# Optimization experiments

Hardware: AMD Instinct MI355X
Metric: run time of the kernel (lower is better)

## Reference

```python
import jax, jax.numpy as jnp
import numpy as np

N = 5
C = 256
B, H, W = 8, 64, 64


def setup_inputs() -> dict:
    key = jax.random.key(0)
    ks = jax.random.split(key, 9)
    s = 0.05
    return {
        "inputs": jax.random.normal(ks[0], (B, N, C, H, W), dtype=jnp.float32),
        # grouped 1x1 conv: groups = N-1, each group maps C channels -> 1 channel, no bias
        "wgt_w": jax.random.normal(ks[1], (N - 1, C), dtype=jnp.float32) * s,
        # ConvGRU 1x1 gate convs: in = 2*C (cat of input and hidden), out = C, with bias
        "w_r": jax.random.normal(ks[2], (C, 2 * C), dtype=jnp.float32) * s,
        "b_r": jnp.zeros((C,), dtype=jnp.float32),
        "w_u": jax.random.normal(ks[3], (C, 2 * C), dtype=jnp.float32) * s,
        "b_u": jnp.zeros((C,), dtype=jnp.float32),
        "w_o": jax.random.normal(ks[4], (C, 2 * C), dtype=jnp.float32) * s,
        "b_o": jnp.zeros((C,), dtype=jnp.float32),
        "gamma": jax.random.normal(ks[5], (1,), dtype=jnp.float32) * s,
    }


def _conv1x1(x, Wm, bias):
    # x: [b, cin, h, w]; Wm: [cout, cin]
    return jnp.einsum("bchw,oc->bohw", x, Wm) + bias[None, :, None, None]


def reference(inputs, wgt_w, w_r, b_r, w_u, b_u, w_o, b_o, gamma):
    b, n, c, h, w = inputs.shape

    def gru(x, hprev):
        s = jnp.concatenate([x, hprev], axis=1)  # [b, 2c, h, w]
        u = jax.nn.sigmoid(_conv1x1(s, w_u, b_u))
        r = jax.nn.sigmoid(_conv1x1(s, w_r, b_r))
        o = jnp.tanh(_conv1x1(jnp.concatenate([x, hprev * r], axis=1), w_o, b_o))
        return hprev * (1.0 - u) + o * u

    preds = []
    for i in range(n):
        h_t = inputs[:, i]  # [b, c, h, w]
        idx = [j for j in range(n) if j != i]
        h_n = inputs[:, jnp.array(idx)]  # [b, n-1, c, h, w], neighbor-major channel layout
        diff = h_t[:, None] - h_n  # repeat(h_t, n-1) - cat(neighbors)
        # grouped 1x1 conv (groups = n-1, no bias): per-neighbor channel reduction
        wgt = jnp.einsum("bjchw,jc->bjhw", diff, wgt_w)  # [b, n-1, h, w]
        gate = jax.nn.sigmoid(wgt)
        # torch: wgt.unsqueeze(1).repeat(1, c, 1, 1, 1).view(b, c*(n-1), h, w)
        # -> flat channel index = cc*(n-1) + j  (note: differs from x2's j*c + cc layout)
        gate_full = jnp.broadcast_to(gate[:, None], (b, c, n - 1, h, w)).reshape(
            b, c * (n - 1), h, w
        )
        x2 = h_n.reshape(b, (n - 1) * c, h, w)
        msg = x2 * gate_full
        m_t = msg.reshape(b, n - 1, c, h, w).sum(axis=1)  # sum-aggregate over neighbors
        h_new = gru(m_t, h_t)
        preds.append(h_new * gamma + h_t)
    return jnp.stack(preds, axis=1)  # [b, n, c, h, w]
```

## Files before the change

### kernel.cpp

```cpp
#include <hip/hip_runtime.h>

typedef __attribute__((ext_vector_type(8))) short short8;
typedef __attribute__((ext_vector_type(4))) float f32x4;
typedef __attribute__((ext_vector_type(8))) unsigned short us8;
typedef __attribute__((ext_vector_type(4))) unsigned short us4;
typedef __attribute__((ext_vector_type(2))) unsigned short us2;

__device__ __forceinline__ float sigmoidf_(float x){ return 1.f/(1.f+__expf(-x)); }
__device__ __forceinline__ unsigned short f2bf(float f){
    union{float f; unsigned int u;} x; x.f = f;
    unsigned int r = x.u + 0x7fffu + ((x.u>>16)&1u);
    return (unsigned short)(r>>16);
}
__device__ __forceinline__ float bf2f(unsigned short u){
    union{unsigned int u; float f;} x; x.u = ((unsigned int)u)<<16; return x.f;
}
#define GAS(p) ((const __attribute__((address_space(1))) void*)(uintptr_t)(p))
#define LAS(p) ((__attribute__((address_space(3))) void*)(uintptr_t)(p))

#define SLOT 8388608ull

__global__ __launch_bounds__(256) void k_dots(const float* __restrict__ inp, const float* __restrict__ wgt,
                                              float* __restrict__ D){
    __shared__ float wg[1024];
    for (int s=threadIdx.x; s<1024; s+=256) wg[s] = wgt[s];
    __syncthreads();
    int e = blockIdx.x*256 + threadIdx.x;
    int pl = e & 4095;
    int bn = e >> 12;
    const float* base = inp + (((size_t)bn*256)<<12) + pl;
    float d0=0,d1=0,d2=0,d3=0;
    #pragma unroll 8
    for (int c=0;c<256;c++){
        float v = base[(size_t)c<<12];
        d0 += v*wg[c]; d1 += v*wg[256+c]; d2 += v*wg[512+c]; d3 += v*wg[768+c];
    }
    size_t o = ((size_t)bn*4)<<12;
    D[o+pl]=d0; D[o+4096+pl]=d1; D[o+8192+pl]=d2; D[o+12288+pl]=d3;
}

__global__ __launch_bounds__(256) void k_wp2(const float* __restrict__ w_u, const float* __restrict__ w_r,
                                             const float* __restrict__ w_o,
                                             unsigned short* __restrict__ Wc0, unsigned short* __restrict__ Wc1){
    int bx = blockIdx.x;
    const float *s0, *s1; unsigned short* dst; int OCN, tid;
    if (bx < 256){ tid = bx*256 + threadIdx.x; OCN = 512; s0 = w_u; s1 = w_r; dst = Wc0; }
    else         { tid = (bx-256)*256 + threadIdx.x; OCN = 256; s0 = w_o; s1 = w_o; dst = Wc1; }
    int d = tid*4;
    int kk = d & 63;
    int row = d >> 6;
    int oc = row & (OCN-1);
    int kb = row / OCN;
    int k  = kb*64 + kk;
    const float* src = (oc < 256) ? s0 : s1;
    int ocr = (oc < 256) ? oc : oc-256;
    float4 v = *(const float4*)&src[(size_t)ocr*512 + k];
    us4 pk; pk.x=f2bf(v.x); pk.y=f2bf(v.y); pk.z=f2bf(v.z); pk.w=f2bf(v.w);
    int kk_sw = kk ^ ((oc&7)<<3);
    *(us4*)&dst[(size_t)row*64 + kk_sw] = pk;
}

__global__ __launch_bounds__(256) void k_bxs(const float* __restrict__ inp, const float* __restrict__ D,
                                             unsigned short* __restrict__ Alo, unsigned short* __restrict__ Ahi,
                                             int i0, int cnt){
    __shared__ unsigned short tm[64*34];
    __shared__ unsigned short th[64*34];
    int t  = threadIdx.x;
    int c0 = (blockIdx.x & 3) << 6;
    int pz = blockIdx.x >> 2;
    int p0 = pz << 5;
    int b  = p0 >> 12, pl0 = p0 & 4095;

    f32x4 x[5][2], S4[2];
    #pragma unroll
    for (int q=0;q<2;q++){
        int s = t + q*256;
        int c = s >> 3, pc = (s&7) << 2;
        int cc = c0 + c;
        f32x4 acc = {0.f,0.f,0.f,0.f};
        #pragma unroll
        for (int n=0;n<5;n++){
            x[n][q] = *(const f32x4*)&inp[(((size_t)((b*5+n)*256+cc))<<12) + pl0 + pc];
            acc += x[n][q];
        }
        S4[q] = acc;
    }
    int kb = c0 >> 6;
    #pragma unroll
    for (int i=0;i<5;i++){
        if (i < i0 || i >= i0+cnt) continue;
        #pragma unroll
        for (int q=0;q<2;q++){
            int s = t + q*256;
            int c = s >> 3, pc = (s&7) << 2;
            int j = c & 3;
            int node = (j < i) ? j : (j+1);
            f32x4 dw = *(const f32x4*)&D[(((size_t)((b*5+i)*4+j))<<12) + pl0 + pc];
            f32x4 dn = *(const f32x4*)&D[(((size_t)((b*5+node)*4+j))<<12) + pl0 + pc];
            f32x4 xi = x[i][q];
            f32x4 md = S4[q] - xi;
            int lb = c*34 + pc;
            us2 m0, m1, h0, h1;
            m0.x = f2bf(sigmoidf_(dw.x-dn.x)*md.x); m0.y = f2bf(sigmoidf_(dw.y-dn.y)*md.y);
            m1.x = f2bf(sigmoidf_(dw.z-dn.z)*md.z); m1.y = f2bf(sigmoidf_(dw.w-dn.w)*md.w);
            h0.x = f2bf(xi.x); h0.y = f2bf(xi.y); h1.x = f2bf(xi.z); h1.y = f2bf(xi.w);
            *(us2*)&tm[lb] = m0; *(us2*)&tm[lb+2] = m1;
            *(us2*)&th[lb] = h0; *(us2*)&th[lb+2] = h1;
        }
        __syncthreads();
        {
            int p = t >> 3, cs = (t&7) << 3;
            us8 vm, vh;
            #pragma unroll
            for (int j8=0;j8<8;j8++){ vm[j8] = tm[(cs+j8)*34 + p]; vh[j8] = th[(cs+j8)*34 + p]; }
            int cs_sw = cs ^ ((p&7)<<3);
            size_t dst = (size_t)(i - i0)*SLOT + ((size_t)kb*32768 + p0 + p)*64 + cs_sw;
            *(us8*)&Alo[dst] = vm;
            *(us8*)&Ahi[dst] = vh;
        }
        __syncthreads();
    }
}

template<int EPI>
__global__ __launch_bounds__(256) void k_mm(
        const unsigned short* __restrict__ Alo, const unsigned short* __restrict__ Ahi,
        const unsigned short* __restrict__ Wb,
        const float* __restrict__ inp, const float* __restrict__ b0, const float* __restrict__ b1,
        unsigned short* __restrict__ U, unsigned short* __restrict__ A1hi, float* __restrict__ outp,
        const float* __restrict__ gamma_p, int i0)
{
    constexpr int OCN = EPI ? 256 : 512;
    constexpr int NY  = EPI ? 2   : 4;
    constexpr int NWG = 256*NY;
    __shared__ unsigned short As[2][128*64];
    __shared__ unsigned short Bs[2][128*64];
    int t  = threadIdx.x, wv = t>>6, ln = t&63;

    int bid = blockIdx.x;
    int wg  = (bid&7)*(NWG>>3) + (bid>>3);
    int oc0 = (wg & (NY-1)) * 128;
    int p0  = (wg / NY) * 128;

    int z  = blockIdx.z, i = i0 + z;
    size_t zo = (size_t)z*SLOT;
    int wm = (wv>>1)*64, wn = (wv&1)*64;
    int row = ln & 15, quad = ln >> 4, kq = quad*8;

    f32x4 acc[4][4];
    f32x4 zr = {0.f,0.f,0.f,0.f};
    #pragma unroll
    for (int a=0;a<4;a++){
        #pragma unroll
        for (int o=0;o<4;o++) acc[a][o]=zr;
    }

    auto stage = [&](int kb, int buf){
        const unsigned short* gA = (kb<4) ? (Alo + zo + ((size_t)kb*32768 + p0)*64)
                                          : (Ahi + zo + ((size_t)(kb-4)*32768 + p0)*64);
        const unsigned short* gW = Wb + ((size_t)kb*OCN + oc0)*64;
        #pragma unroll
        for (int q=0;q<4;q++){
            int off = (wv*4+q)*512;
            __builtin_amdgcn_global_load_lds(GAS(gA + off + ln*8), LAS(&Bs[buf][off + ln*8]), 16, 0, 0);
            __builtin_amdgcn_global_load_lds(GAS(gW + off + ln*8), LAS(&As[buf][off + ln*8]), 16, 0, 0);
        }
    };

    stage(0, 0);
    __syncthreads();

    int rsw = (row&7)<<3;
    for (int kb=0; kb<8; ++kb){
        int cur = kb & 1;
        if (kb < 7) stage(kb+1, cur^1);
        #pragma unroll
        for (int ks=0; ks<2; ks++){
            short8 a[4], b[4];
            int col = (ks*32 + kq) ^ rsw;
            #pragma unroll
            for (int f=0; f<4; f++){
                a[f] = *(const short8*)&As[cur][(wm+f*16+row)*64 + col];
                b[f] = *(const short8*)&Bs[cur][(wn+f*16+row)*64 + col];
            }
            __builtin_amdgcn_s_setprio(1);
            #pragma unroll
            for (int fm=0; fm<4; fm++){
                #pragma unroll
                for (int fn=0; fn<4; fn++)
                    acc[fm][fn] = __builtin_amdgcn_mfma_f32_16x16x32_bf16(a[fm], b[fn], acc[fm][fn], 0,0,0);
            }
            __builtin_amdgcn_s_setprio(0);
        }
        __syncthreads();
    }

    float gm = EPI ? gamma_p[0] : 0.f;
    #pragma unroll
    for (int fn=0; fn<4; fn++){
        int p  = p0 + wn + fn*16 + row;
        int b  = p >> 12, pl = p & 4095;
        size_t hb = (((size_t)((b*5+i)*256))<<12) + pl;
        #pragma unroll
        for (int fm=0; fm<4; fm++){
            int ocb = oc0 + wm + fm*16 + quad*4;
            if (EPI==0){
                if (oc0 < 256){
                    us4 pk;
                    #pragma unroll
                    for (int r=0;r<4;r++)
                        pk[r] = f2bf(sigmoidf_(acc[fm][fn][r] + b0[ocb+r]));
                    *(us4*)&U[zo + (size_t)p*256 + ocb] = pk;
                } else {
                    int kb2 = ocb - 256;
                    int kc  = (kb2&63) ^ ((p&7)<<3);
                    size_t aidx = zo + ((size_t)(kb2>>6)*32768 + p)*64 + kc;
                    us4 vh = *(const us4*)&Ahi[aidx];
                    us4 pk;
                    #pragma unroll
                    for (int r=0;r<4;r++){
                        float rg = sigmoidf_(acc[fm][fn][r] + b1[kb2+r]);
                        pk[r] = f2bf(rg * bf2f(vh[r]));
                    }
                    *(us4*)&A1hi[aidx] = pk;
                }
            } else {
                us4 vu = *(const us4*)&U[zo + (size_t)p*256 + ocb];
                #pragma unroll
                for (int r=0;r<4;r++){
                    int oc = ocb + r;
                    float v  = acc[fm][fn][r] + b0[oc];
                    float e2 = __expf(2.f*v);
                    float thv = 1.f - 2.f/(e2+1.f);
                    float u  = bf2f(vu[r]);
                    float h  = inp[hb + ((size_t)oc<<12)];
                    float hn = h*(1.f-u) + thv*u;
                    outp[hb + ((size_t)oc<<12)] = hn*gm + h;
                }
            }
        }
    }
}

extern "C" void kernel_launch(void* const* d_in, const int* in_sizes, int n_in,
                              void* d_out, int out_size, void* d_ws, size_t ws_size,
                              hipStream_t stream) {
    const float* inputs = (const float*)d_in[0];
    const float* wgt_w  = (const float*)d_in[1];
    const float* w_r    = (const float*)d_in[2];
    const float* b_r    = (const float*)d_in[3];
    const float* w_u    = (const float*)d_in[4];
    const float* b_u    = (const float*)d_in[5];
    const float* w_o    = (const float*)d_in[6];
    const float* b_o    = (const float*)d_in[7];
    const float* gamma  = (const float*)d_in[8];
    float* out = (float*)d_out;

    float* D = (float*)d_ws;
    unsigned short* Wc0 = (unsigned short*)(D + 655360);
    unsigned short* Wc1 = Wc0 + 262144;
    unsigned short* U   = Wc1 + 131072;

    size_t fixedB = 655360ull*4 + (262144ull + 131072ull)*2;
    size_t slotB  = 4ull*SLOT*2;
    int nb = 1;
    for (int k2=5;k2>=1;k2--){ if (fixedB + (size_t)k2*slotB <= ws_size){ nb = k2; break; } }

    unsigned short* Alo  = U   + (size_t)nb*SLOT;
    unsigned short* Ahi  = Alo + (size_t)nb*SLOT;
    unsigned short* A1hi = Ahi + (size_t)nb*SLOT;

    k_dots<<<640, 256, 0, stream>>>(inputs, wgt_w, D);
    k_wp2 <<<384, 256, 0, stream>>>(w_u, w_r, w_o, Wc0, Wc1);
    for (int i0=0; i0<5; i0+=nb){
        int cnt = (5-i0 < nb) ? (5-i0) : nb;
        k_bxs<<<4096, 256, 0, stream>>>(inputs, D, Alo, Ahi, i0, cnt);
        k_mm<0><<<dim3(1024,1,cnt), 256, 0, stream>>>(Alo, Ahi, Wc0, inputs, b_u, b_r,
                                                      U, A1hi, nullptr, gamma, i0);
        k_mm<1><<<dim3(512,1,cnt), 256, 0, stream>>>(Alo, A1hi, Wc1, inputs, b_o, nullptr,
                                                     U, nullptr, out, gamma, i0);
    }
}
```

Before: 707.6 us.

## Fuse gate dot products into message builder and make GEMMs persistent

Removes the separate k_dots kernel: each message-building block now computes the per-pixel neighbor dot products for its 32 pixels in shared memory before building the bf16 operand tiles, eliminating the D workspace round trip. Each block now covers all four channel tiles of its pixels, so the grid shrinks from 4096 to 1024 blocks. The GEMM kernels become persistent with 256 blocks, each looping over several output tiles with a 3-stage global-to-LDS pipeline using explicit vmcnt waits and running the epilogue inside the loop. The U intermediate uses a tile-contiguous layout for coalesced epilogue stores. This trades launch overhead and extra memory traffic for recomputing the dot products per node in every block, higher LDS use per block, and fewer resident blocks.

New measurement: 753.5 us. 1.06x slower.

```diff
diff --git a/kernel.cpp b/kernel.cpp
--- a/kernel.cpp
+++ b/kernel.cpp
@@ -19,25 +19,6 @@
 #define LAS(p) ((__attribute__((address_space(3))) void*)(uintptr_t)(p))
 
 #define SLOT 8388608ull
-
-__global__ __launch_bounds__(256) void k_dots(const float* __restrict__ inp, const float* __restrict__ wgt,
-                                              float* __restrict__ D){
-    __shared__ float wg[1024];
-    for (int s=threadIdx.x; s<1024; s+=256) wg[s] = wgt[s];
-    __syncthreads();
-    int e = blockIdx.x*256 + threadIdx.x;
-    int pl = e & 4095;
-    int bn = e >> 12;
-    const float* base = inp + (((size_t)bn*256)<<12) + pl;
-    float d0=0,d1=0,d2=0,d3=0;
-    #pragma unroll 8
-    for (int c=0;c<256;c++){
-        float v = base[(size_t)c<<12];
-        d0 += v*wg[c]; d1 += v*wg[256+c]; d2 += v*wg[512+c]; d3 += v*wg[768+c];
-    }
-    size_t o = ((size_t)bn*4)<<12;
-    D[o+pl]=d0; D[o+4096+pl]=d1; D[o+8192+pl]=d2; D[o+12288+pl]=d3;
-}
 
 __global__ __launch_bounds__(256) void k_wp2(const float* __restrict__ w_u, const float* __restrict__ w_r,
                                              const float* __restrict__ w_o,
@@ -60,65 +41,95 @@
     *(us4*)&dst[(size_t)row*64 + kk_sw] = pk;
 }
 
-__global__ __launch_bounds__(256) void k_bxs(const float* __restrict__ inp, const float* __restrict__ D,
-                                             unsigned short* __restrict__ Alo, unsigned short* __restrict__ Ahi,
-                                             int i0, int cnt){
+__global__ __launch_bounds__(256) void k_bxsd(const float* __restrict__ inp, const float* __restrict__ wgt,
+                                              unsigned short* __restrict__ Alo, unsigned short* __restrict__ Ahi,
+                                              int i0, int cnt){
+    __shared__ float wg[1024];
+    __shared__ float dpart[8*640];
+    __shared__ float Dl[640];
     __shared__ unsigned short tm[64*34];
     __shared__ unsigned short th[64*34];
     int t  = threadIdx.x;
-    int c0 = (blockIdx.x & 3) << 6;
-    int pz = blockIdx.x >> 2;
-    int p0 = pz << 5;
+    int p0 = blockIdx.x << 5;
     int b  = p0 >> 12, pl0 = p0 & 4095;
-
-    f32x4 x[5][2], S4[2];
-    #pragma unroll
-    for (int q=0;q<2;q++){
-        int s = t + q*256;
-        int c = s >> 3, pc = (s&7) << 2;
-        int cc = c0 + c;
-        f32x4 acc = {0.f,0.f,0.f,0.f};
-        #pragma unroll
-        for (int n=0;n<5;n++){
-            x[n][q] = *(const f32x4*)&inp[(((size_t)((b*5+n)*256+cc))<<12) + pl0 + pc];
-            acc += x[n][q];
-        }
-        S4[q] = acc;
-    }
-    int kb = c0 >> 6;
-    #pragma unroll
-    for (int i=0;i<5;i++){
-        if (i < i0 || i >= i0+cnt) continue;
+    for (int s=t; s<1024; s+=256) wg[s] = wgt[s];
+    __syncthreads();
+    {
+        int px = t & 31, cg = t >> 5;
+        float d[20];
+        #pragma unroll
+        for (int o=0;o<20;o++) d[o]=0.f;
+        #pragma unroll
+        for (int cc=0; cc<32; cc++){
+            int c = cg*32 + cc;
+            float w0 = wg[c], w1 = wg[256+c], w2 = wg[512+c], w3 = wg[768+c];
+            #pragma unroll
+            for (int n=0;n<5;n++){
+                float v = inp[(((size_t)((b*5+n)*256+c))<<12) + pl0 + px];
+                d[n*4+0] += v*w0; d[n*4+1] += v*w1; d[n*4+2] += v*w2; d[n*4+3] += v*w3;
+            }
+        }
+        #pragma unroll
+        for (int o=0;o<20;o++) dpart[cg*640 + o*32 + px] = d[o];
+    }
+    __syncthreads();
+    for (int o=t; o<640; o+=256){
+        float s = 0.f;
+        #pragma unroll
+        for (int g=0; g<8; g++) s += dpart[g*640 + o];
+        Dl[o] = s;
+    }
+    __syncthreads();
+    for (int ct=0; ct<4; ct++){
+        int c0 = ct << 6;
+        f32x4 x[5][2], S4[2];
         #pragma unroll
         for (int q=0;q<2;q++){
             int s = t + q*256;
             int c = s >> 3, pc = (s&7) << 2;
-            int j = c & 3;
-            int node = (j < i) ? j : (j+1);
-            f32x4 dw = *(const f32x4*)&D[(((size_t)((b*5+i)*4+j))<<12) + pl0 + pc];
-            f32x4 dn = *(const f32x4*)&D[(((size_t)((b*5+node)*4+j))<<12) + pl0 + pc];
-            f32x4 xi = x[i][q];
-            f32x4 md = S4[q] - xi;
-            int lb = c*34 + pc;
-            us2 m0, m1, h0, h1;
-            m0.x = f2bf(sigmoidf_(dw.x-dn.x)*md.x); m0.y = f2bf(sigmoidf_(dw.y-dn.y)*md.y);
-            m1.x = f2bf(sigmoidf_(dw.z-dn.z)*md.z); m1.y = f2bf(sigmoidf_(dw.w-dn.w)*md.w);
-            h0.x = f2bf(xi.x); h0.y = f2bf(xi.y); h1.x = f2bf(xi.z); h1.y = f2bf(xi.w);
-            *(us2*)&tm[lb] = m0; *(us2*)&tm[lb+2] = m1;
-            *(us2*)&th[lb] = h0; *(us2*)&th[lb+2] = h1;
-        }
-        __syncthreads();
-        {
-            int p = t >> 3, cs = (t&7) << 3;
-            us8 vm, vh;
-            #pragma unroll
-            for (int j8=0;j8<8;j8++){ vm[j8] = tm[(cs+j8)*34 + p]; vh[j8] = th[(cs+j8)*34 + p]; }
-            int cs_sw = cs ^ ((p&7)<<3);
-            size_t dst = (size_t)(i - i0)*SLOT + ((size_t)kb*32768 + p0 + p)*64 + cs_sw;
-            *(us8*)&Alo[dst] = vm;
-            *(us8*)&Ahi[dst] = vh;
-        }
-        __syncthreads();
+            int cc = c0 + c;
+            f32x4 acc = {0.f,0.f,0.f,0.f};
+            #pragma unroll
+            for (int n=0;n<5;n++){
+                x[n][q] = *(const f32x4*)&inp[(((size_t)((b*5+n)*256+cc))<<12) + pl0 + pc];
+                acc += x[n][q];
+            }
+            S4[q] = acc;
+        }
+        #pragma unroll
+        for (int i=0;i<5;i++){
+            if (i < i0 || i >= i0+cnt) continue;
+            #pragma unroll
+            for (int q=0;q<2;q++){
+                int s = t + q*256;
+                int c = s >> 3, pc = (s&7) << 2;
+                int j = c & 3;
+                int node = (j < i) ? j : (j+1);
+                f32x4 dw = *(const f32x4*)&Dl[(i*4+j)*32 + pc];
+                f32x4 dn = *(const f32x4*)&Dl[(node*4+j)*32 + pc];
+                f32x4 xi = x[i][q];
+                f32x4 md = S4[q] - xi;
+                int lb = c*34 + pc;
+                us2 m0, m1, h0, h1;
+                m0.x = f2bf(sigmoidf_(dw.x-dn.x)*md.x); m0.y = f2bf(sigmoidf_(dw.y-dn.y)*md.y);
+                m1.x = f2bf(sigmoidf_(dw.z-dn.z)*md.z); m1.y = f2bf(sigmoidf_(dw.w-dn.w)*md.w);
+                h0.x = f2bf(xi.x); h0.y = f2bf(xi.y); h1.x = f2bf(xi.z); h1.y = f2bf(xi.w);
+                *(us2*)&tm[lb] = m0; *(us2*)&tm[lb+2] = m1;
+                *(us2*)&th[lb] = h0; *(us2*)&th[lb+2] = h1;
+            }
+            __syncthreads();
+            {
+                int p = t >> 3, cs = (t&7) << 3;
+                us8 vm, vh;
+                #pragma unroll
+                for (int j8=0;j8<8;j8++){ vm[j8] = tm[(cs+j8)*34 + p]; vh[j8] = th[(cs+j8)*34 + p]; }
+                int cs_sw = cs ^ ((p&7)<<3);
+                size_t dst = (size_t)(i - i0)*SLOT + ((size_t)ct*32768 + p0 + p)*64 + cs_sw;
+                *(us8*)&Alo[dst] = vm;
+                *(us8*)&Ahi[dst] = vh;
+            }
+            __syncthreads();
+        }
     }
 }
 
@@ -128,24 +139,22 @@
         const unsigned short* __restrict__ Wb,
         const float* __restrict__ inp, const float* __restrict__ b0, const float* __restrict__ b1,
         unsigned short* __restrict__ U, unsigned short* __restrict__ A1hi, float* __restrict__ outp,
-        const float* __restrict__ gamma_p, int i0)
+        const float* __restrict__ gamma_p, int i0, int cnt)
 {
     constexpr int OCN = EPI ? 256 : 512;
     constexpr int NY  = EPI ? 2   : 4;
-    constexpr int NWG = 256*NY;
-    __shared__ unsigned short As[2][128*64];
-    __shared__ unsigned short Bs[2][128*64];
+    __shared__ unsigned short As[3][128*64];
+    __shared__ unsigned short Bs[3][128*64];
     int t  = threadIdx.x, wv = t>>6, ln = t&63;
-
-    int bid = blockIdx.x;
-    int wg  = (bid&7)*(NWG>>3) + (bid>>3);
-    int oc0 = (wg & (NY-1)) * 128;
-    int p0  = (wg / NY) * 128;
-
-    int z  = blockIdx.z, i = i0 + z;
-    size_t zo = (size_t)z*SLOT;
+    int NU = 256*NY*cnt;
+    int NS = (NU >> 8) * 8;
+    int chunk = blockIdx.x >> 5, k_in = blockIdx.x & 31;
+    int ubase = chunk*(NU>>3) + k_in;
+    int oc0 = (ubase & (NY-1)) * 128;
     int wm = (wv>>1)*64, wn = (wv&1)*64;
     int row = ln & 15, quad = ln >> 4, kq = quad*8;
+    int rsw = (row&7)<<3;
+    float gm = EPI ? gamma_p[0] : 0.f;
 
     f32x4 acc[4][4];
     f32x4 zr = {0.f,0.f,0.f,0.f};
@@ -155,10 +164,17 @@
         for (int o=0;o<4;o++) acc[a][o]=zr;
     }
 
-    auto stage = [&](int kb, int buf){
-        const unsigned short* gA = (kb<4) ? (Alo + zo + ((size_t)kb*32768 + p0)*64)
-                                          : (Ahi + zo + ((size_t)(kb-4)*32768 + p0)*64);
+    auto stage = [&](int s){
+        if (s >= NS) return;
+        int u  = ubase + (s>>3)*32;
+        int pz = u / NY;
+        int kb = s & 7;
+        int p0s = (pz & 255) << 7;
+        size_t zos = (size_t)(pz >> 8) * SLOT;
+        const unsigned short* gA = (kb<4) ? (Alo + zos + ((size_t)kb*32768 + p0s)*64)
+                                          : (Ahi + zos + ((size_t)(kb-4)*32768 + p0s)*64);
         const unsigned short* gW = Wb + ((size_t)kb*OCN + oc0)*64;
+        int buf = s % 3;
         #pragma unroll
         for (int q=0;q<4;q++){
             int off = (wv*4+q)*512;
@@ -167,13 +183,14 @@
         }
     };
 
-    stage(0, 0);
-    __syncthreads();
-
-    int rsw = (row&7)<<3;
-    for (int kb=0; kb<8; ++kb){
-        int cur = kb & 1;
-        if (kb < 7) stage(kb+1, cur^1);
+    stage(0); stage(1);
+    for (int s=0; s<NS; ++s){
+        if (s+1 < NS) { asm volatile("s_waitcnt vmcnt(8)" ::: "memory"); }
+        else          { asm volatile("s_waitcnt vmcnt(0)" ::: "memory"); }
+        __builtin_amdgcn_s_barrier();
+        __builtin_amdgcn_sched_barrier(0);
+        stage(s+2);
+        const int cur = s % 3;
         #pragma unroll
         for (int ks=0; ks<2; ks++){
             short8 a[4], b[4];
@@ -183,60 +200,85 @@
                 a[f] = *(const short8*)&As[cur][(wm+f*16+row)*64 + col];
                 b[f] = *(const short8*)&Bs[cur][(wn+f*16+row)*64 + col];
             }
-            __builtin_amdgcn_s_setprio(1);
             #pragma unroll
             for (int fm=0; fm<4; fm++){
                 #pragma unroll
                 for (int fn=0; fn<4; fn++)
                     acc[fm][fn] = __builtin_amdgcn_mfma_f32_16x16x32_bf16(a[fm], b[fn], acc[fm][fn], 0,0,0);
             }
-            __builtin_amdgcn_s_setprio(0);
-        }
-        __syncthreads();
-    }
-
-    float gm = EPI ? gamma_p[0] : 0.f;
-    #pragma unroll
-    for (int fn=0; fn<4; fn++){
-        int p  = p0 + wn + fn*16 + row;
-        int b  = p >> 12, pl = p & 4095;
-        size_t hb = (((size_t)((b*5+i)*256))<<12) + pl;
-        #pragma unroll
-        for (int fm=0; fm<4; fm++){
-            int ocb = oc0 + wm + fm*16 + quad*4;
+        }
+        if ((s&7)==7){
+            int u  = ubase + (s>>3)*32;
+            int pz = u / NY;
+            int p0 = (pz & 255) << 7;
+            int z  = pz >> 8;
+            size_t zo = (size_t)z*SLOT;
+            int i  = i0 + z;
             if (EPI==0){
                 if (oc0 < 256){
-                    us4 pk;
+                    size_t ub = zo + (size_t)((p0>>7)*2 + (oc0>>7))*16384 + (size_t)t*4;
                     #pragma unroll
-                    for (int r=0;r<4;r++)
-                        pk[r] = f2bf(sigmoidf_(acc[fm][fn][r] + b0[ocb+r]));
-                    *(us4*)&U[zo + (size_t)p*256 + ocb] = pk;
+                    for (int fn=0; fn<4; fn++){
+                        #pragma unroll
+                        for (int fm=0; fm<4; fm++){
+                            int ocb = oc0 + wm + fm*16 + quad*4;
+                            us4 pk;
+                            #pragma unroll
+                            for (int r=0;r<4;r++)
+                                pk[r] = f2bf(sigmoidf_(acc[fm][fn][r] + b0[ocb+r]));
+                            *(us4*)&U[ub + (size_t)(fn*4+fm)*1024] = pk;
+                        }
+                    }
                 } else {
-                    int kb2 = ocb - 256;
-                    int kc  = (kb2&63) ^ ((p&7)<<3);
-                    size_t aidx = zo + ((size_t)(kb2>>6)*32768 + p)*64 + kc;
-                    us4 vh = *(const us4*)&Ahi[aidx];
-                    us4 pk;
                     #pragma unroll
-                    for (int r=0;r<4;r++){
-                        float rg = sigmoidf_(acc[fm][fn][r] + b1[kb2+r]);
-                        pk[r] = f2bf(rg * bf2f(vh[r]));
+                    for (int fn=0; fn<4; fn++){
+                        int p = p0 + wn + fn*16 + row;
+                        #pragma unroll
+                        for (int fm=0; fm<4; fm++){
+                            int ocb = oc0 + wm + fm*16 + quad*4;
+                            int kb2 = ocb - 256;
+                            int kc  = (kb2&63) ^ ((p&7)<<3);
+                            size_t aidx = zo + ((size_t)(kb2>>6)*32768 + p)*64 + kc;
+                            us4 vh = *(const us4*)&Ahi[aidx];
+                            us4 pk;
+                            #pragma unroll
+                            for (int r=0;r<4;r++){
+                                float rg = sigmoidf_(acc[fm][fn][r] + b1[kb2+r]);
+                                pk[r] = f2bf(rg * bf2f(vh[r]));
+                            }
+                            *(us4*)&A1hi[aidx] = pk;
+                        }
                     }
-                    *(us4*)&A1hi[aidx] = pk;
                 }
             } else {
-                us4 vu = *(const us4*)&U[zo + (size_t)p*256 + ocb];
+                size_t ub = zo + (size_t)((p0>>7)*2 + (oc0>>7))*16384 + (size_t)t*4;
                 #pragma unroll
-                for (int r=0;r<4;r++){
-                    int oc = ocb + r;
-                    float v  = acc[fm][fn][r] + b0[oc];
-                    float e2 = __expf(2.f*v);
-                    float thv = 1.f - 2.f/(e2+1.f);
-                    float u  = bf2f(vu[r]);
-                    float h  = inp[hb + ((size_t)oc<<12)];
-                    float hn = h*(1.f-u) + thv*u;
-                    outp[hb + ((size_t)oc<<12)] = hn*gm + h;
+                for (int fn=0; fn<4; fn++){
+                    int p  = p0 + wn + fn*16 + row;
+                    int b  = p >> 12, pl = p & 4095;
+                    size_t hb = (((size_t)((b*5+i)*256))<<12) + pl;
+                    #pragma unroll
+                    for (int fm=0; fm<4; fm++){
+                        int ocb = oc0 + wm + fm*16 + quad*4;
+                        us4 vu = *(const us4*)&U[ub + (size_t)(fn*4+fm)*1024];
+                        #pragma unroll
+                        for (int r=0;r<4;r++){
+                            int oc = ocb + r;
+                            float v  = acc[fm][fn][r] + b0[oc];
+                            float e2 = __expf(2.f*v);
+                            float thv = 1.f - 2.f/(e2+1.f);
+                            float uu = bf2f(vu[r]);
+                            float h  = inp[hb + ((size_t)oc<<12)];
+                            float hn = h*(1.f-uu) + thv*uu;
+                            outp[hb + ((size_t)oc<<12)] = hn*gm + h;
+                        }
+                    }
                 }
+            }
+            #pragma unroll
+            for (int a2=0;a2<4;a2++){
+                #pragma unroll
+                for (int o2=0;o2<4;o2++) acc[a2][o2]=zr;
             }
         }
     }
@@ -256,12 +298,11 @@
     const float* gamma  = (const float*)d_in[8];
     float* out = (float*)d_out;
 
-    float* D = (float*)d_ws;
-    unsigned short* Wc0 = (unsigned short*)(D + 655360);
+    unsigned short* Wc0 = (unsigned short*)d_ws;
     unsigned short* Wc1 = Wc0 + 262144;
     unsigned short* U   = Wc1 + 131072;
 
-    size_t fixedB = 655360ull*4 + (262144ull + 131072ull)*2;
+    size_t fixedB = (262144ull + 131072ull)*2;
     size_t slotB  = 4ull*SLOT*2;
     int nb = 1;
     for (int k2=5;k2>=1;k2--){ if (fixedB + (size_t)k2*slotB <= ws_size){ nb = k2; break; } }
@@ -270,14 +311,13 @@
     unsigned short* Ahi  = Alo + (size_t)nb*SLOT;
     unsigned short* A1hi = Ahi + (size_t)nb*SLOT;
 
-    k_dots<<<640, 256, 0, stream>>>(inputs, wgt_w, D);
     k_wp2 <<<384, 256, 0, stream>>>(w_u, w_r, w_o, Wc0, Wc1);
     for (int i0=0; i0<5; i0+=nb){
         int cnt = (5-i0 < nb) ? (5-i0) : nb;
-        k_bxs<<<4096, 256, 0, stream>>>(inputs, D, Alo, Ahi, i0, cnt);
-        k_mm<0><<<dim3(1024,1,cnt), 256, 0, stream>>>(Alo, Ahi, Wc0, inputs, b_u, b_r,
-                                                      U, A1hi, nullptr, gamma, i0);
-        k_mm<1><<<dim3(512,1,cnt), 256, 0, stream>>>(Alo, A1hi, Wc1, inputs, b_o, nullptr,
-                                                     U, nullptr, out, gamma, i0);
-    }
-}
+        k_bxsd<<<1024, 256, 0, stream>>>(inputs, wgt_w, Alo, Ahi, i0, cnt);
+        k_mm<0><<<256, 256, 0, stream>>>(Alo, Ahi, Wc0, inputs, b_u, b_r,
+                                         U, A1hi, nullptr, gamma, i0, cnt);
+        k_mm<1><<<256, 256, 0, stream>>>(Alo, A1hi, Wc1, inputs, b_o, nullptr,
+                                         U, nullptr, out, gamma, i0, cnt);
+    }
+}
```
